# Performance work log

Measured on AMD Instinct MI355X. Metric: run time of the kernel, lower is better.

The kernel has to match this reference:

```python
import jax, jax.numpy as jnp
import numpy as np

S, B, D = 2048, 2, 1024   # seq_len, batch, d_model
H, Dh = 16, 64            # n_head, d_head (H*Dh == D)
LN_EPS = 1e-5


def _rel_shift(x):
    # x: [qlen, klen, bsz, n_head] -- standard Transformer-XL relative shift
    q, k, b, n = x.shape
    x = jnp.pad(x, ((0, 0), (1, 0), (0, 0), (0, 0)))  # [q, k+1, b, n]
    x = x.reshape(k + 1, q, b, n)[1:]                  # drop first row
    return x.reshape(q, k, b, n)


def setup_inputs() -> dict:
    key = jax.random.key(0)
    ks = jax.random.split(key, 8)
    s = 0.02
    return {
        "x":    jax.random.normal(ks[0], (S, B, D), jnp.float32),
        "r":    jax.random.normal(ks[1], (1, D), jnp.float32),          # learned pos vector
        "rw":   jax.random.normal(ks[2], (H, Dh), jnp.float32),          # content bias
        "rr":   jax.random.normal(ks[3], (H, Dh), jnp.float32),          # position bias
        "ln_g": jnp.ones((D,), jnp.float32),
        "ln_b": jnp.zeros((D,), jnp.float32),
        "Wqkv": jax.random.normal(ks[4], (D, 3 * H * Dh), jnp.float32) * s,
        "Wr":   jax.random.normal(ks[5], (D, H * Dh), jnp.float32) * s,
        "Wo":   jax.random.normal(ks[6], (H * Dh, D), jnp.float32) * s,
    }


def reference(x, r, rw, rr, ln_g, ln_b, Wqkv, Wr, Wo):
    # Pre-LayerNorm (dropout = identity in eval mode)
    mu = jnp.mean(x, axis=-1, keepdims=True)
    var = jnp.mean(jnp.square(x - mu), axis=-1, keepdims=True)
    xn = (x - mu) * jax.lax.rsqrt(var + LN_EPS) * ln_g + ln_b   # [S,B,D]

    # relative position input: r expanded over seq
    r_exp = jnp.broadcast_to(r, (S, D))                          # [S,D]

    qkv = xn @ Wqkv                                              # [S,B,3*H*Dh]
    q, k, v = jnp.split(qkv, 3, axis=-1)
    q = q.reshape(S, B, H, Dh)
    k = k.reshape(S, B, H, Dh)
    v = v.reshape(S, B, H, Dh)
    rk = (r_exp @ Wr).reshape(S, H, Dh)                          # [S,H,Dh]

    scale = 1.0 / np.sqrt(Dh).astype(np.float32)
    AC = jnp.einsum('ibnd,jbnd->ijbn', q + rw, k)                # content term
    BD = jnp.einsum('ibnd,jnd->ijbn', q + rr, rk)                # position term
    BD = _rel_shift(BD)
    attn = jax.nn.softmax((AC + BD) * scale, axis=1)             # over key axis j

    av = jnp.einsum('ijbn,jbnd->ibnd', attn, v).reshape(S, B, H * Dh)
    return xn + av @ Wo                                          # residual w/ normed input
```

## Files before the change

kernel.cpp:

```cpp
#include <hip/hip_runtime.h>

typedef unsigned short u16;
typedef __attribute__((ext_vector_type(8))) __bf16 bf16x8;
typedef __attribute__((ext_vector_type(8))) u16 u16x8;
typedef __attribute__((ext_vector_type(4))) float f32x4;
typedef __attribute__((ext_vector_type(16))) float f32x16;

__device__ __forceinline__ float bf2f(u16 u){
  union { unsigned int i; float f; } v; v.i = ((unsigned int)u) << 16; return v.f;
}
__device__ __forceinline__ u16 f2bf(float f){
  union { float f; unsigned int u; } v; v.f = f;
  unsigned int u = v.u;
  u += 0x7FFFu + ((u >> 16) & 1u);
  return (u16)(u >> 16);
}
__device__ __forceinline__ unsigned fbits(float f){
  union { float f; unsigned u; } v; v.f = f; return v.u;
}
__device__ __forceinline__ void gld_lds16(const u16* g, u16* l){
  __builtin_amdgcn_global_load_lds((const __attribute__((address_space(1))) unsigned int*)g,
                                   (__attribute__((address_space(3))) unsigned int*)l, 16, 0, 0);
}

__global__ __launch_bounds__(256) void prep_k(const float* __restrict__ Wqkv, u16* __restrict__ wqkvT,
                                              const float* __restrict__ Wo, u16* __restrict__ woT,
                                              const float* __restrict__ r, const float* __restrict__ Wr,
                                              float* __restrict__ rk0,
                                              const float* __restrict__ x, const float* __restrict__ gw,
                                              const float* __restrict__ bw, u16* __restrict__ xnb){
  __shared__ float tile[32][33];
  __shared__ float red[8];
  const int tx = threadIdx.x, ty = threadIdx.y;
  const int t = ty * 32 + tx;
  if(blockIdx.x == 128){
    const int n = blockIdx.y * 32 + (t & 31);
    const int chunk = t >> 5;
    float acc = 0.f;
    const int d0 = chunk * 128;
    for(int d = d0; d < d0 + 128; ++d)
      acc += r[d] * Wr[(size_t)d * 1024 + n];
    tile[chunk][t & 31] = acc;
    __syncthreads();
    if(chunk == 0){
      float s = 0.f;
      #pragma unroll
      for(int c = 0; c < 8; ++c) s += tile[c][t & 31];
      rk0[n] = s;
    }
    return;
  }
  if(blockIdx.x >= 129){
    const int row = (blockIdx.x - 129) * 32 + blockIdx.y;
    const float* xr = x + (size_t)row * 1024;
    float4 xv = *reinterpret_cast<const float4*>(xr + t * 4);
    float s  = xv.x + xv.y + xv.z + xv.w;
    float s2 = xv.x*xv.x + xv.y*xv.y + xv.z*xv.z + xv.w*xv.w;
    #pragma unroll
    for(int m = 1; m <= 32; m <<= 1){ s += __shfl_xor(s, m, 64); s2 += __shfl_xor(s2, m, 64); }
    const int w = t >> 6, lane = t & 63;
    if(lane == 0){ red[w] = s; red[4 + w] = s2; }
    __syncthreads();
    float S1 = red[0] + red[1] + red[2] + red[3];
    float S2 = red[4] + red[5] + red[6] + red[7];
    float mu = S1 * (1.f/1024.f);
    float var = S2 * (1.f/1024.f) - mu * mu;
    float rstd = rsqrtf(var + 1e-5f);
    float4 gv = *reinterpret_cast<const float4*>(gw + t * 4);
    float4 bv = *reinterpret_cast<const float4*>(bw + t * 4);
    ushort4 o;
    o.x = f2bf((xv.x - mu) * rstd * gv.x + bv.x);
    o.y = f2bf((xv.y - mu) * rstd * gv.y + bv.y);
    o.z = f2bf((xv.z - mu) * rstd * gv.z + bv.z);
    o.w = f2bf((xv.w - mu) * rstd * gv.w + bv.w);
    *reinterpret_cast<ushort4*>(xnb + (size_t)row * 1024 + t * 4) = o;
    return;
  }
  const float* in; u16* out; int C, bxx;
  if(blockIdx.x < 96){ in = Wqkv; out = wqkvT; C = 3072; bxx = blockIdx.x; }
  else               { in = Wo;   out = woT;   C = 1024; bxx = blockIdx.x - 96; }
  const int bx = bxx * 32, by = blockIdx.y * 32;
  #pragma unroll
  for(int i = 0; i < 32; i += 8)
    tile[ty + i][tx] = in[(size_t)(by + ty + i) * C + bx + tx];
  __syncthreads();
  #pragma unroll
  for(int i = 0; i < 32; i += 8)
    out[(size_t)(bx + ty + i) * 1024 + by + tx] = f2bf(tile[tx][ty + i]);
}

__global__ __launch_bounds__(256) void gemm_qkv_k(const u16* __restrict__ A, const u16* __restrict__ BT,
                                                  u16* __restrict__ Cb, u16* __restrict__ vT){
  __shared__ u16 sA[2][128 * 32];
  __shared__ u16 sB[2][128 * 32];
  __shared__ u16 tl[128 * 66];
  const int t = threadIdx.x;
  const int row0 = blockIdx.y * 128, col0 = blockIdx.x * 128;
  const int w = t >> 6, lane = t & 63, g = lane >> 4, lq = lane & 15;
  const int wr = (w >> 1) * 64, wc = (w & 1) * 64;
  const int K = 1024;
  f32x4 zero4 = {0.f, 0.f, 0.f, 0.f};
  f32x4 acc[4][4];
  #pragma unroll
  for(int mi = 0; mi < 4; ++mi)
    #pragma unroll
    for(int ni = 0; ni < 4; ++ni) acc[mi][ni] = zero4;

  for(int kt = 0; kt < K; kt += 64){
    #pragma unroll
    for(int ks = 0; ks < 2; ++ks){
      const int kk = kt + ks * 32;
      gld_lds16(A  + (size_t)(row0 +      (t >> 2)) * K + kk + (t & 3) * 8, &sA[ks][w * 512]);
      gld_lds16(A  + (size_t)(row0 + 64 + (t >> 2)) * K + kk + (t & 3) * 8, &sA[ks][2048 + w * 512]);
      gld_lds16(BT + (size_t)(col0 +      (t >> 2)) * K + kk + (t & 3) * 8, &sB[ks][w * 512]);
      gld_lds16(BT + (size_t)(col0 + 64 + (t >> 2)) * K + kk + (t & 3) * 8, &sB[ks][2048 + w * 512]);
    }
    __syncthreads();
    #pragma unroll
    for(int ks = 0; ks < 2; ++ks){
      bf16x8 af[4];
      #pragma unroll
      for(int mi = 0; mi < 4; ++mi)
        af[mi] = *reinterpret_cast<const bf16x8*>(&sA[ks][(wr + mi * 16 + lq) * 32 + g * 8]);
      #pragma unroll
      for(int ni = 0; ni < 4; ++ni){
        bf16x8 bfr = *reinterpret_cast<const bf16x8*>(&sB[ks][(wc + ni * 16 + lq) * 32 + g * 8]);
        #pragma unroll
        for(int mi = 0; mi < 4; ++mi)
          acc[mi][ni] = __builtin_amdgcn_mfma_f32_16x16x32_bf16(af[mi], bfr, acc[mi][ni], 0, 0, 0);
      }
    }
    __syncthreads();
  }
  if(blockIdx.x < 16){
    #pragma unroll
    for(int mi = 0; mi < 4; ++mi)
      #pragma unroll
      for(int ni = 0; ni < 4; ++ni)
        #pragma unroll
        for(int rg = 0; rg < 4; ++rg){
          const int row = row0 + wr + mi * 16 + g * 4 + rg;
          const int col = col0 + wc + ni * 16 + lq;
          Cb[(size_t)row * 2048 + col] = f2bf(acc[mi][ni][rg]);
        }
  } else {
    const int cv0 = col0 - 2048;
    #pragma unroll
    for(int half = 0; half < 2; ++half){
      if((w & 1) == half){
        #pragma unroll
        for(int mi = 0; mi < 4; ++mi)
          #pragma unroll
          for(int ni = 0; ni < 4; ++ni)
            #pragma unroll
            for(int rg = 0; rg < 4; ++rg)
              tl[(wr + mi * 16 + g * 4 + rg) * 66 + ni * 16 + lq] = f2bf(acc[mi][ni][rg]);
      }
      __syncthreads();
      const int h = (cv0 >> 6) + half;
      const int b2 = w >> 1, dup = w & 1, d = lane;
      const int R = (b2 * 16 + h) * 64 + d;
      u16 tmp[32];
      #pragma unroll
      for(int e = 0; e < 32; ++e)
        tmp[e] = tl[((dup * 32 + e) * 2 + b2) * 66 + d];
      u16* op = vT + (size_t)R * 2048 + (row0 >> 1) + dup * 32;
      *reinterpret_cast<u16x8*>(op)      = *reinterpret_cast<u16x8*>(&tmp[0]);
      *reinterpret_cast<u16x8*>(op + 8)  = *reinterpret_cast<u16x8*>(&tmp[8]);
      *reinterpret_cast<u16x8*>(op + 16) = *reinterpret_cast<u16x8*>(&tmp[16]);
      *reinterpret_cast<u16x8*>(op + 24) = *reinterpret_cast<u16x8*>(&tmp[24]);
      __syncthreads();
    }
  }
}

__global__ __launch_bounds__(256) void gemm_out_k(const u16* __restrict__ A, const u16* __restrict__ BT,
                                                  const u16* __restrict__ res, float* __restrict__ Cf){
  __shared__ u16 sA[128 * 32];
  __shared__ u16 sB[64 * 32];
  const int t = threadIdx.x;
  const int row0 = blockIdx.y * 128, col0 = blockIdx.x * 64;
  const int w = t >> 6, lane = t & 63, g = lane >> 4, lq = lane & 15;
  const int wr = (w >> 1) * 64, wc = (w & 1) * 32;
  const int K = 1024, N = 1024;
  f32x4 zero4 = {0.f, 0.f, 0.f, 0.f};
  f32x4 acc[4][2];
  #pragma unroll
  for(int mi = 0; mi < 4; ++mi)
    #pragma unroll
    for(int ni = 0; ni < 2; ++ni) acc[mi][ni] = zero4;

  for(int kt = 0; kt < K; kt += 32){
    gld_lds16(A  + (size_t)(row0 +      (t >> 2)) * K + kt + (t & 3) * 8, &sA[w * 512]);
    gld_lds16(A  + (size_t)(row0 + 64 + (t >> 2)) * K + kt + (t & 3) * 8, &sA[2048 + w * 512]);
    gld_lds16(BT + (size_t)(col0 +      (t >> 2)) * K + kt + (t & 3) * 8, &sB[w * 512]);
    __syncthreads();
    bf16x8 af[4];
    #pragma unroll
    for(int mi = 0; mi < 4; ++mi)
      af[mi] = *reinterpret_cast<const bf16x8*>(&sA[(wr + mi * 16 + lq) * 32 + g * 8]);
    #pragma unroll
    for(int ni = 0; ni < 2; ++ni){
      bf16x8 bfr = *reinterpret_cast<const bf16x8*>(&sB[(wc + ni * 16 + lq) * 32 + g * 8]);
      #pragma unroll
      for(int mi = 0; mi < 4; ++mi)
        acc[mi][ni] = __builtin_amdgcn_mfma_f32_16x16x32_bf16(af[mi], bfr, acc[mi][ni], 0, 0, 0);
    }
    __syncthreads();
  }
  #pragma unroll
  for(int mi = 0; mi < 4; ++mi)
    #pragma unroll
    for(int ni = 0; ni < 2; ++ni)
      #pragma unroll
      for(int rg = 0; rg < 4; ++rg){
        const int row = row0 + wr + mi * 16 + g * 4 + rg;
        const int col = col0 + wc + ni * 16 + lq;
        Cf[(size_t)row * N + col] = acc[mi][ni][rg] + bf2f(res[(size_t)row * N + col]);
      }
}

__global__ __launch_bounds__(256) void attn_k(const u16* __restrict__ qk, const u16* __restrict__ vT,
                                              const float* __restrict__ rw, const float* __restrict__ rr,
                                              const float* __restrict__ rk0, u16* __restrict__ av){
  constexpr int S = 2048, ST = 74;
  __shared__ u16 ks[2][64 * ST];
  __shared__ u16 vs[2][64 * ST];
  const int t = threadIdx.x;
  const int i0 = blockIdx.x * 128;
  const int bh = blockIdx.y;
  const int b = bh >> 4, h = bh & 15;
  const int w = t >> 6, lane = t & 63, m = lane & 31, q5 = lane >> 5;
  const int iw0 = i0 + w * 32;
  const int i_lane = iw0 + m;
  const float SC = 0.125f * 1.4426950408889634f;

  bf16x8 qf[4];
  float ciL, cpL;
  {
    const bool hasnext = (i_lane + 1 < S);
    const u16* qp  = qk + (size_t)(i_lane * 2 + b) * 2048 + h * 64;
    const u16* qp2 = qk + (size_t)((hasnext ? i_lane + 1 : i_lane) * 2 + b) * 2048 + h * 64;
    const float* rwp = rw  + h * 64;
    const float* rrp = rr  + h * 64;
    const float* rkp = rk0 + h * 64;
    float cpart = 0.f, cppart = 0.f;
    #pragma unroll
    for(int kt = 0; kt < 4; ++kt){
      const int dbase = kt * 16 + q5 * 8;
      u16x8 qv  = *reinterpret_cast<const u16x8*>(qp  + dbase);
      u16x8 qv2 = *reinterpret_cast<const u16x8*>(qp2 + dbase);
      u16x8 a;
      #pragma unroll
      for(int e = 0; e < 8; ++e){
        const float qe  = bf2f(qv[e]);
        const float rke = rkp[dbase + e];
        const float rre = rrp[dbase + e];
        a[e] = f2bf((qe + rwp[dbase + e]) * SC);
        cpart  += (qe + rre) * rke;
        cppart += (bf2f(qv2[e]) + rre) * rke;
      }
      qf[kt] = *reinterpret_cast<bf16x8*>(&a);
    }
    cpart  += __shfl_xor(cpart, 32, 64);
    cppart += __shfl_xor(cppart, 32, 64);
    ciL = cpart * SC;
    cpL = hasnext ? cppart * SC : 0.0f;
  }

  f32x16 acc0, acc1, z16;
  #pragma unroll
  for(int e = 0; e < 16; ++e) z16[e] = 0.f;
  acc0 = z16; acc1 = z16;
  float rsum = 0.f;

  const int jr = t >> 2, c0 = (t & 3) * 16;
  {
    const u16* kp = qk + (size_t)(jr * 2 + b) * 2048 + 1024 + h * 64 + c0;
    *reinterpret_cast<u16x8*>(&ks[0][jr * ST + c0])     = *reinterpret_cast<const u16x8*>(kp);
    *reinterpret_cast<u16x8*>(&ks[0][jr * ST + c0 + 8]) = *reinterpret_cast<const u16x8*>(kp + 8);
    const u16* vp = vT + ((size_t)bh * 64 + jr) * 2048 + c0;
    *reinterpret_cast<u16x8*>(&vs[0][jr * ST + c0])     = *reinterpret_cast<const u16x8*>(vp);
    *reinterpret_cast<u16x8*>(&vs[0][jr * ST + c0 + 8]) = *reinterpret_cast<const u16x8*>(vp + 8);
  }
  __syncthreads();

  for(int n = 0; n < 32; ++n){
    const int p = n & 1;
    u16x8 k0, k1, v0, v1;
    const bool pre = (n + 1 < 32);
    if(pre){
      const int j0n = (n + 1) * 64;
      const u16* kp = qk + (size_t)((j0n + jr) * 2 + b) * 2048 + 1024 + h * 64 + c0;
      k0 = *reinterpret_cast<const u16x8*>(kp);
      k1 = *reinterpret_cast<const u16x8*>(kp + 8);
      const u16* vp = vT + ((size_t)bh * 64 + jr) * 2048 + j0n + c0;
      v0 = *reinterpret_cast<const u16x8*>(vp);
      v1 = *reinterpret_cast<const u16x8*>(vp + 8);
    }
    const int j0 = n * 64;
    bf16x8 pfrag[4];
    #pragma unroll
    for(int jt = 0; jt < 2; ++jt){
      const int tj0 = j0 + jt * 32;
      f32x16 s = z16;
      #pragma unroll
      for(int kt = 0; kt < 4; ++kt){
        bf16x8 ka = *reinterpret_cast<const bf16x8*>(&ks[p][(jt * 32 + m) * ST + kt * 16 + q5 * 8]);
        s = __builtin_amdgcn_mfma_f32_32x32x16_bf16(ka, qf[kt], s, 0, 0, 0);
      }
      float pv[16];
      if(tj0 + 31 <= iw0){
        #pragma unroll
        for(int r2 = 0; r2 < 16; ++r2) pv[r2] = __builtin_amdgcn_exp2f(s[r2] + ciL);
      } else if(tj0 >= iw0 + 33){
        #pragma unroll
        for(int r2 = 0; r2 < 16; ++r2) pv[r2] = __builtin_amdgcn_exp2f(s[r2] + cpL);
      } else {
        #pragma unroll
        for(int r2 = 0; r2 < 16; ++r2){
          const int j = tj0 + (r2 & 3) + 8 * (r2 >> 2) + 4 * q5;
          const float t1 = (j <= i_lane) ? ciL : cpL;
          const float bdL = (j == i_lane + 1) ? 0.0f : t1;
          pv[r2] = __builtin_amdgcn_exp2f(s[r2] + bdL);
        }
      }
      #pragma unroll
      for(int r2 = 0; r2 < 16; ++r2) rsum += pv[r2];
      unsigned pk[8];
      #pragma unroll
      for(int q = 0; q < 8; ++q)
        pk[q] = __builtin_amdgcn_perm(fbits(pv[2 * q + 1]), fbits(pv[2 * q]), 0x07060302);
      unsigned sAx = (q5 == 0) ? pk[2] : pk[0];
      unsigned sAy = (q5 == 0) ? pk[3] : pk[1];
      unsigned rAx = (unsigned)__shfl_xor((int)sAx, 32, 64);
      unsigned rAy = (unsigned)__shfl_xor((int)sAy, 32, 64);
      unsigned sBx = (q5 == 0) ? pk[6] : pk[4];
      unsigned sBy = (q5 == 0) ? pk[7] : pk[5];
      unsigned rBx = (unsigned)__shfl_xor((int)sBx, 32, 64);
      unsigned rBy = (unsigned)__shfl_xor((int)sBy, 32, 64);
      union { unsigned u[4]; bf16x8 bf; } f0, f1;
      if(q5 == 0){
        f0.u[0] = pk[0]; f0.u[1] = pk[1]; f0.u[2] = rAx; f0.u[3] = rAy;
        f1.u[0] = pk[4]; f1.u[1] = pk[5]; f1.u[2] = rBx; f1.u[3] = rBy;
      } else {
        f0.u[0] = rAx; f0.u[1] = rAy; f0.u[2] = pk[2]; f0.u[3] = pk[3];
        f1.u[0] = rBx; f1.u[1] = rBy; f1.u[2] = pk[6]; f1.u[3] = pk[7];
      }
      pfrag[jt * 2 + 0] = f0.bf;
      pfrag[jt * 2 + 1] = f1.bf;
    }
    #pragma unroll
    for(int kt = 0; kt < 4; ++kt){
      bf16x8 va0 = *reinterpret_cast<const bf16x8*>(&vs[p][(m) * ST + kt * 16 + q5 * 8]);
      acc0 = __builtin_amdgcn_mfma_f32_32x32x16_bf16(va0, pfrag[kt], acc0, 0, 0, 0);
      bf16x8 va1 = *reinterpret_cast<const bf16x8*>(&vs[p][(32 + m) * ST + kt * 16 + q5 * 8]);
      acc1 = __builtin_amdgcn_mfma_f32_32x32x16_bf16(va1, pfrag[kt], acc1, 0, 0, 0);
    }
    if(pre){
      const int q2 = p ^ 1;
      *reinterpret_cast<u16x8*>(&ks[q2][jr * ST + c0])     = k0;
      *reinterpret_cast<u16x8*>(&ks[q2][jr * ST + c0 + 8]) = k1;
      *reinterpret_cast<u16x8*>(&vs[q2][jr * ST + c0])     = v0;
      *reinterpret_cast<u16x8*>(&vs[q2][jr * ST + c0 + 8]) = v1;
    }
    __syncthreads();
  }
  rsum += __shfl_xor(rsum, 32, 64);
  const float rinv = 1.0f / rsum;
  u16* op = av + (size_t)(i_lane * 2 + b) * 1024 + h * 64;
  #pragma unroll
  for(int dt = 0; dt < 2; ++dt){
    const f32x16& A = dt ? acc1 : acc0;
    #pragma unroll
    for(int rq = 0; rq < 4; ++rq){
      ushort4 o;
      o.x = f2bf(A[rq * 4 + 0] * rinv);
      o.y = f2bf(A[rq * 4 + 1] * rinv);
      o.z = f2bf(A[rq * 4 + 2] * rinv);
      o.w = f2bf(A[rq * 4 + 3] * rinv);
      const int d0 = dt * 32 + 8 * rq + 4 * q5;
      *reinterpret_cast<ushort4*>(op + d0) = o;
    }
  }
}

extern "C" void kernel_launch(void* const* d_in, const int* in_sizes, int n_in,
                              void* d_out, int out_size, void* d_ws, size_t ws_size,
                              hipStream_t stream){
  (void)in_sizes; (void)n_in; (void)out_size; (void)ws_size;
  const float* x    = (const float*)d_in[0];
  const float* r    = (const float*)d_in[1];
  const float* rw   = (const float*)d_in[2];
  const float* rr   = (const float*)d_in[3];
  const float* ln_g = (const float*)d_in[4];
  const float* ln_b = (const float*)d_in[5];
  const float* Wqkv = (const float*)d_in[6];
  const float* Wr   = (const float*)d_in[7];
  const float* Wo   = (const float*)d_in[8];
  char* ws = (char*)d_ws;
  u16*   xnb   = (u16*)(ws + 0);
  u16*   qk    = (u16*)(ws + 8388608);
  u16*   av    = (u16*)(ws + 25165824);
  u16*   woT   = (u16*)(ws + 33554432);
  u16*   wqkvT = (u16*)(ws + 35651584);
  u16*   vT    = (u16*)(ws + 41943040);
  float* rk0   = (float*)(ws + 50331648);
  float* out   = (float*)d_out;

  prep_k<<<dim3(257, 32), dim3(32, 8), 0, stream>>>(Wqkv, wqkvT, Wo, woT, r, Wr, rk0,
                                                    x, ln_g, ln_b, xnb);
  gemm_qkv_k<<<dim3(24, 32), 256, 0, stream>>>(xnb, wqkvT, qk, vT);
  attn_k<<<dim3(16, 32), 256, 0, stream>>>(qk, vT, rw, rr, rk0, av);
  gemm_out_k<<<dim3(16, 32), 256, 0, stream>>>(av, woT, xnb, out);
}
```

Before: 224.7 us.

## Split attention key range across two wave groups with LDS reduction

Doubles the attention block to 512 threads, with pairs of waves sharing the same 32 query rows and each handling alternate 64-key tiles. Partial accumulators and row sums from the odd-tile waves are combined through shared memory before normalisation. The aim is more waves in flight per query tile, giving better latency hiding and MFMA utilisation on a grid of only 512 blocks. In exchange, the double-buffered prefetch becomes a single buffer with an extra barrier per iteration, and there is a reduction step at the end.

```diff
diff --git a/kernel.cpp b/kernel.cpp
--- a/kernel.cpp
+++ b/kernel.cpp
@@ -220,18 +220,18 @@
       }
 }
 
-__global__ __launch_bounds__(256) void attn_k(const u16* __restrict__ qk, const u16* __restrict__ vT,
-                                              const float* __restrict__ rw, const float* __restrict__ rr,
-                                              const float* __restrict__ rk0, u16* __restrict__ av){
+__global__ __launch_bounds__(512, 4) void attn_k(const u16* __restrict__ qk, const u16* __restrict__ vT,
+                                                 const float* __restrict__ rw, const float* __restrict__ rr,
+                                                 const float* __restrict__ rk0, u16* __restrict__ av){
   constexpr int S = 2048, ST = 74;
-  __shared__ u16 ks[2][64 * ST];
-  __shared__ u16 vs[2][64 * ST];
+  __shared__ u16 smem[4][64 * ST];
   const int t = threadIdx.x;
   const int i0 = blockIdx.x * 128;
   const int bh = blockIdx.y;
   const int b = bh >> 4, h = bh & 15;
   const int w = t >> 6, lane = t & 63, m = lane & 31, q5 = lane >> 5;
-  const int iw0 = i0 + w * 32;
+  const int qw = w >> 1, kw = w & 1;
+  const int iw0 = i0 + qw * 32;
   const int i_lane = iw0 + m;
   const float SC = 0.125f * 1.4426950408889634f;
 
@@ -274,31 +274,34 @@
   acc0 = z16; acc1 = z16;
   float rsum = 0.f;
 
-  const int jr = t >> 2, c0 = (t & 3) * 16;
+  const int jr = t >> 3, c0 = (t & 7) * 8;
+  const int lo = jr * ST + c0;
   {
     const u16* kp = qk + (size_t)(jr * 2 + b) * 2048 + 1024 + h * 64 + c0;
-    *reinterpret_cast<u16x8*>(&ks[0][jr * ST + c0])     = *reinterpret_cast<const u16x8*>(kp);
-    *reinterpret_cast<u16x8*>(&ks[0][jr * ST + c0 + 8]) = *reinterpret_cast<const u16x8*>(kp + 8);
+    *reinterpret_cast<u16x8*>(&smem[0][lo]) = *reinterpret_cast<const u16x8*>(kp);
+    *reinterpret_cast<u16x8*>(&smem[1][lo]) = *reinterpret_cast<const u16x8*>(kp + (size_t)64 * 2 * 2048);
     const u16* vp = vT + ((size_t)bh * 64 + jr) * 2048 + c0;
-    *reinterpret_cast<u16x8*>(&vs[0][jr * ST + c0])     = *reinterpret_cast<const u16x8*>(vp);
-    *reinterpret_cast<u16x8*>(&vs[0][jr * ST + c0 + 8]) = *reinterpret_cast<const u16x8*>(vp + 8);
+    *reinterpret_cast<u16x8*>(&smem[2][lo]) = *reinterpret_cast<const u16x8*>(vp);
+    *reinterpret_cast<u16x8*>(&smem[3][lo]) = *reinterpret_cast<const u16x8*>(vp + 64);
   }
   __syncthreads();
 
-  for(int n = 0; n < 32; ++n){
-    const int p = n & 1;
-    u16x8 k0, k1, v0, v1;
-    const bool pre = (n + 1 < 32);
+  const u16* ksb = &smem[kw][0];
+  const u16* vsb = &smem[2 + kw][0];
+
+  for(int np = 0; np < 16; ++np){
+    u16x8 kE, kO, vE, vO;
+    const bool pre = (np + 1 < 16);
     if(pre){
-      const int j0n = (n + 1) * 64;
+      const int j0n = (2 * np + 2) * 64;
       const u16* kp = qk + (size_t)((j0n + jr) * 2 + b) * 2048 + 1024 + h * 64 + c0;
-      k0 = *reinterpret_cast<const u16x8*>(kp);
-      k1 = *reinterpret_cast<const u16x8*>(kp + 8);
+      kE = *reinterpret_cast<const u16x8*>(kp);
+      kO = *reinterpret_cast<const u16x8*>(kp + (size_t)64 * 2 * 2048);
       const u16* vp = vT + ((size_t)bh * 64 + jr) * 2048 + j0n + c0;
-      v0 = *reinterpret_cast<const u16x8*>(vp);
-      v1 = *reinterpret_cast<const u16x8*>(vp + 8);
-    }
-    const int j0 = n * 64;
+      vE = *reinterpret_cast<const u16x8*>(vp);
+      vO = *reinterpret_cast<const u16x8*>(vp + 64);
+    }
+    const int j0 = (2 * np + kw) * 64;
     bf16x8 pfrag[4];
     #pragma unroll
     for(int jt = 0; jt < 2; ++jt){
@@ -306,7 +309,7 @@
       f32x16 s = z16;
       #pragma unroll
       for(int kt = 0; kt < 4; ++kt){
-        bf16x8 ka = *reinterpret_cast<const bf16x8*>(&ks[p][(jt * 32 + m) * ST + kt * 16 + q5 * 8]);
+        bf16x8 ka = *reinterpret_cast<const bf16x8*>(&ksb[(jt * 32 + m) * ST + kt * 16 + q5 * 8]);
         s = __builtin_amdgcn_mfma_f32_32x32x16_bf16(ka, qf[kt], s, 0, 0, 0);
       }
       float pv[16];
@@ -352,35 +355,53 @@
     }
     #pragma unroll
     for(int kt = 0; kt < 4; ++kt){
-      bf16x8 va0 = *reinterpret_cast<const bf16x8*>(&vs[p][(m) * ST + kt * 16 + q5 * 8]);
+      bf16x8 va0 = *reinterpret_cast<const bf16x8*>(&vsb[(m) * ST + kt * 16 + q5 * 8]);
       acc0 = __builtin_amdgcn_mfma_f32_32x32x16_bf16(va0, pfrag[kt], acc0, 0, 0, 0);
-      bf16x8 va1 = *reinterpret_cast<const bf16x8*>(&vs[p][(32 + m) * ST + kt * 16 + q5 * 8]);
+      bf16x8 va1 = *reinterpret_cast<const bf16x8*>(&vsb[(32 + m) * ST + kt * 16 + q5 * 8]);
       acc1 = __builtin_amdgcn_mfma_f32_32x32x16_bf16(va1, pfrag[kt], acc1, 0, 0, 0);
     }
+    __syncthreads();
     if(pre){
-      const int q2 = p ^ 1;
-      *reinterpret_cast<u16x8*>(&ks[q2][jr * ST + c0])     = k0;
-      *reinterpret_cast<u16x8*>(&ks[q2][jr * ST + c0 + 8]) = k1;
-      *reinterpret_cast<u16x8*>(&vs[q2][jr * ST + c0])     = v0;
-      *reinterpret_cast<u16x8*>(&vs[q2][jr * ST + c0 + 8]) = v1;
-    }
-    __syncthreads();
-  }
+      *reinterpret_cast<u16x8*>(&smem[0][lo]) = kE;
+      *reinterpret_cast<u16x8*>(&smem[1][lo]) = kO;
+      *reinterpret_cast<u16x8*>(&smem[2][lo]) = vE;
+      *reinterpret_cast<u16x8*>(&smem[3][lo]) = vO;
+    }
+    __syncthreads();
+  }
+
   rsum += __shfl_xor(rsum, 32, 64);
-  const float rinv = 1.0f / rsum;
-  u16* op = av + (size_t)(i_lane * 2 + b) * 1024 + h * 64;
-  #pragma unroll
-  for(int dt = 0; dt < 2; ++dt){
-    const f32x16& A = dt ? acc1 : acc0;
-    #pragma unroll
-    for(int rq = 0; rq < 4; ++rq){
-      ushort4 o;
-      o.x = f2bf(A[rq * 4 + 0] * rinv);
-      o.y = f2bf(A[rq * 4 + 1] * rinv);
-      o.z = f2bf(A[rq * 4 + 2] * rinv);
-      o.w = f2bf(A[rq * 4 + 3] * rinv);
-      const int d0 = dt * 32 + 8 * rq + 4 * q5;
-      *reinterpret_cast<ushort4*>(op + d0) = o;
+
+  float* com = reinterpret_cast<float*>(&smem[0][0]) + (size_t)(qw * 64 + lane) * 33;
+  if(kw == 1){
+    #pragma unroll
+    for(int e = 0; e < 16; ++e) com[e] = acc0[e];
+    #pragma unroll
+    for(int e = 0; e < 16; ++e) com[16 + e] = acc1[e];
+    com[32] = rsum;
+  }
+  __syncthreads();
+  if(kw == 0){
+    #pragma unroll
+    for(int e = 0; e < 16; ++e) acc0[e] += com[e];
+    #pragma unroll
+    for(int e = 0; e < 16; ++e) acc1[e] += com[16 + e];
+    rsum += com[32];
+    const float rinv = 1.0f / rsum;
+    u16* op = av + (size_t)(i_lane * 2 + b) * 1024 + h * 64;
+    #pragma unroll
+    for(int dt = 0; dt < 2; ++dt){
+      const f32x16& A = dt ? acc1 : acc0;
+      #pragma unroll
+      for(int rq = 0; rq < 4; ++rq){
+        ushort4 o;
+        o.x = f2bf(A[rq * 4 + 0] * rinv);
+        o.y = f2bf(A[rq * 4 + 1] * rinv);
+        o.z = f2bf(A[rq * 4 + 2] * rinv);
+        o.w = f2bf(A[rq * 4 + 3] * rinv);
+        const int d0 = dt * 32 + 8 * rq + 4 * q5;
+        *reinterpret_cast<ushort4*>(op + d0) = o;
+      }
     }
   }
 }
@@ -411,6 +432,6 @@
   prep_k<<<dim3(257, 32), dim3(32, 8), 0, stream>>>(Wqkv, wqkvT, Wo, woT, r, Wr, rk0,
                                                     x, ln_g, ln_b, xnb);
   gemm_qkv_k<<<dim3(24, 32), 256, 0, stream>>>(xnb, wqkvT, qk, vT);
-  attn_k<<<dim3(16, 32), 256, 0, stream>>>(qk, vT, rw, rr, rk0, av);
+  attn_k<<<dim3(16, 32), 512, 0, stream>>>(qk, vT, rw, rr, rk0, av);
   gemm_out_k<<<dim3(16, 32), 256, 0, stream>>>(av, woT, xnb, out);
 }
```

Measured after the change: 315.3 us. 40.3% more time.

## Split attention key range across two blocks and combine partials in a separate kernel

Applied to the files above, without the earlier changes.

The attention kernel now takes a third grid dimension that splits the 32 key tiles into two halves. Each half writes unnormalised fp32 partial outputs and row sums to workspace, and a new comb_k kernel adds them, normalises and converts to bf16. The goal is to double the number of blocks so the GPU is better filled and latency is better hidden. The cost is extra global traffic for the fp32 partials, one more kernel launch, and an added __syncthreads per iteration. The split path only runs when the workspace is large enough.

```diff
diff --git a/kernel.cpp b/kernel.cpp
--- a/kernel.cpp
+++ b/kernel.cpp
@@ -222,13 +222,17 @@
 
 __global__ __launch_bounds__(256) void attn_k(const u16* __restrict__ qk, const u16* __restrict__ vT,
                                               const float* __restrict__ rw, const float* __restrict__ rr,
-                                              const float* __restrict__ rk0, u16* __restrict__ av){
+                                              const float* __restrict__ rk0, u16* __restrict__ av,
+                                              float* __restrict__ avp, float* __restrict__ rs){
   constexpr int S = 2048, ST = 74;
   __shared__ u16 ks[2][64 * ST];
   __shared__ u16 vs[2][64 * ST];
   const int t = threadIdx.x;
   const int i0 = blockIdx.x * 128;
   const int bh = blockIdx.y;
+  const int z = blockIdx.z;
+  const bool split = (gridDim.z == 2);
+  const int n0 = z * 16, nt = split ? 16 : 32;
   const int b = bh >> 4, h = bh & 15;
   const int w = t >> 6, lane = t & 63, m = lane & 31, q5 = lane >> 5;
   const int iw0 = i0 + w * 32;
@@ -276,19 +280,19 @@
 
   const int jr = t >> 2, c0 = (t & 3) * 16;
   {
-    const u16* kp = qk + (size_t)(jr * 2 + b) * 2048 + 1024 + h * 64 + c0;
+    const u16* kp = qk + (size_t)((n0 * 64 + jr) * 2 + b) * 2048 + 1024 + h * 64 + c0;
     *reinterpret_cast<u16x8*>(&ks[0][jr * ST + c0])     = *reinterpret_cast<const u16x8*>(kp);
     *reinterpret_cast<u16x8*>(&ks[0][jr * ST + c0 + 8]) = *reinterpret_cast<const u16x8*>(kp + 8);
-    const u16* vp = vT + ((size_t)bh * 64 + jr) * 2048 + c0;
+    const u16* vp = vT + ((size_t)bh * 64 + jr) * 2048 + n0 * 64 + c0;
     *reinterpret_cast<u16x8*>(&vs[0][jr * ST + c0])     = *reinterpret_cast<const u16x8*>(vp);
     *reinterpret_cast<u16x8*>(&vs[0][jr * ST + c0 + 8]) = *reinterpret_cast<const u16x8*>(vp + 8);
   }
   __syncthreads();
 
-  for(int n = 0; n < 32; ++n){
+  for(int n = n0; n < n0 + nt; ++n){
     const int p = n & 1;
     u16x8 k0, k1, v0, v1;
-    const bool pre = (n + 1 < 32);
+    const bool pre = (n + 1 < n0 + nt);
     if(pre){
       const int j0n = (n + 1) * 64;
       const u16* kp = qk + (size_t)((j0n + jr) * 2 + b) * 2048 + 1024 + h * 64 + c0;
@@ -357,6 +361,7 @@
       bf16x8 va1 = *reinterpret_cast<const bf16x8*>(&vs[p][(32 + m) * ST + kt * 16 + q5 * 8]);
       acc1 = __builtin_amdgcn_mfma_f32_32x32x16_bf16(va1, pfrag[kt], acc1, 0, 0, 0);
     }
+    __syncthreads();
     if(pre){
       const int q2 = p ^ 1;
       *reinterpret_cast<u16x8*>(&ks[q2][jr * ST + c0])     = k0;
@@ -367,28 +372,63 @@
     __syncthreads();
   }
   rsum += __shfl_xor(rsum, 32, 64);
-  const float rinv = 1.0f / rsum;
-  u16* op = av + (size_t)(i_lane * 2 + b) * 1024 + h * 64;
-  #pragma unroll
-  for(int dt = 0; dt < 2; ++dt){
-    const f32x16& A = dt ? acc1 : acc0;
-    #pragma unroll
-    for(int rq = 0; rq < 4; ++rq){
-      ushort4 o;
-      o.x = f2bf(A[rq * 4 + 0] * rinv);
-      o.y = f2bf(A[rq * 4 + 1] * rinv);
-      o.z = f2bf(A[rq * 4 + 2] * rinv);
-      o.w = f2bf(A[rq * 4 + 3] * rinv);
-      const int d0 = dt * 32 + 8 * rq + 4 * q5;
-      *reinterpret_cast<ushort4*>(op + d0) = o;
-    }
-  }
+  if(split){
+    float* op = avp + (size_t)z * 4194304 + ((size_t)(i_lane * 2 + b) * 16 + h) * 64;
+    #pragma unroll
+    for(int dt = 0; dt < 2; ++dt){
+      const f32x16& A = dt ? acc1 : acc0;
+      #pragma unroll
+      for(int rq = 0; rq < 4; ++rq){
+        float4 o;
+        o.x = A[rq * 4 + 0]; o.y = A[rq * 4 + 1]; o.z = A[rq * 4 + 2]; o.w = A[rq * 4 + 3];
+        const int d0 = dt * 32 + 8 * rq + 4 * q5;
+        *reinterpret_cast<float4*>(op + d0) = o;
+      }
+    }
+    if(q5 == 0) rs[(size_t)z * 65536 + (size_t)(i_lane * 2 + b) * 16 + h] = rsum;
+  } else {
+    const float rinv = 1.0f / rsum;
+    u16* op = av + (size_t)(i_lane * 2 + b) * 1024 + h * 64;
+    #pragma unroll
+    for(int dt = 0; dt < 2; ++dt){
+      const f32x16& A = dt ? acc1 : acc0;
+      #pragma unroll
+      for(int rq = 0; rq < 4; ++rq){
+        ushort4 o;
+        o.x = f2bf(A[rq * 4 + 0] * rinv);
+        o.y = f2bf(A[rq * 4 + 1] * rinv);
+        o.z = f2bf(A[rq * 4 + 2] * rinv);
+        o.w = f2bf(A[rq * 4 + 3] * rinv);
+        const int d0 = dt * 32 + 8 * rq + 4 * q5;
+        *reinterpret_cast<ushort4*>(op + d0) = o;
+      }
+    }
+  }
+}
+
+__global__ __launch_bounds__(256) void comb_k(const float* __restrict__ avp, const float* __restrict__ rs,
+                                              u16* __restrict__ av){
+  const int gid = blockIdx.x * 256 + threadIdx.x;
+  const size_t i8 = (size_t)gid * 8;
+  const size_t rowh = i8 >> 6;
+  const float rinv = 1.0f / (rs[rowh] + rs[65536 + rowh]);
+  const float4 a0 = *reinterpret_cast<const float4*>(avp + i8);
+  const float4 a1 = *reinterpret_cast<const float4*>(avp + i8 + 4);
+  const float4 b0 = *reinterpret_cast<const float4*>(avp + 4194304 + i8);
+  const float4 b1 = *reinterpret_cast<const float4*>(avp + 4194304 + i8 + 4);
+  ushort4 o0, o1;
+  o0.x = f2bf((a0.x + b0.x) * rinv); o0.y = f2bf((a0.y + b0.y) * rinv);
+  o0.z = f2bf((a0.z + b0.z) * rinv); o0.w = f2bf((a0.w + b0.w) * rinv);
+  o1.x = f2bf((a1.x + b1.x) * rinv); o1.y = f2bf((a1.y + b1.y) * rinv);
+  o1.z = f2bf((a1.z + b1.z) * rinv); o1.w = f2bf((a1.w + b1.w) * rinv);
+  *reinterpret_cast<ushort4*>(av + i8)     = o0;
+  *reinterpret_cast<ushort4*>(av + i8 + 4) = o1;
 }
 
 extern "C" void kernel_launch(void* const* d_in, const int* in_sizes, int n_in,
                               void* d_out, int out_size, void* d_ws, size_t ws_size,
                               hipStream_t stream){
-  (void)in_sizes; (void)n_in; (void)out_size; (void)ws_size;
+  (void)in_sizes; (void)n_in; (void)out_size;
   const float* x    = (const float*)d_in[0];
   const float* r    = (const float*)d_in[1];
   const float* rw   = (const float*)d_in[2];
@@ -406,11 +446,19 @@
   u16*   wqkvT = (u16*)(ws + 35651584);
   u16*   vT    = (u16*)(ws + 41943040);
   float* rk0   = (float*)(ws + 50331648);
+  float* rs    = (float*)(ws + 50335744);
+  float* avp   = (float*)(ws + 50860032);
   float* out   = (float*)d_out;
+  const bool split = ws_size >= (size_t)84414464;
 
   prep_k<<<dim3(257, 32), dim3(32, 8), 0, stream>>>(Wqkv, wqkvT, Wo, woT, r, Wr, rk0,
                                                     x, ln_g, ln_b, xnb);
   gemm_qkv_k<<<dim3(24, 32), 256, 0, stream>>>(xnb, wqkvT, qk, vT);
-  attn_k<<<dim3(16, 32), 256, 0, stream>>>(qk, vT, rw, rr, rk0, av);
+  if(split){
+    attn_k<<<dim3(16, 32, 2), 256, 0, stream>>>(qk, vT, rw, rr, rk0, av, avp, rs);
+    comb_k<<<dim3(2048), 256, 0, stream>>>(avp, rs, av);
+  } else {
+    attn_k<<<dim3(16, 32, 1), 256, 0, stream>>>(qk, vT, rw, rr, rk0, av, avp, rs);
+  }
   gemm_out_k<<<dim3(16, 32), 256, 0, stream>>>(av, woT, xnb, out);
 }
```

After: 235.2 us. +4.7%, slower.

## Software-pipeline attention: overlap next tile QK^T/softmax with current PV MFMAs

Applied to the files above, without the earlier changes.

Restructures the attention inner loop so the QK^T scores and softmax of tile n+1 are computed while the PV MFMAs of tile n issue. Global K/V loads now prefetch two tiles ahead, which needs an extra barrier per iteration before the LDS buffer is overwritten. It also adds a launch-bounds occupancy hint of 2 blocks per SM. The aim is to hide exp and softmax latency behind matrix work, at the cost of more live registers and an extra __syncthreads.

```diff
diff --git a/kernel.cpp b/kernel.cpp
--- a/kernel.cpp
+++ b/kernel.cpp
@@ -220,9 +220,9 @@
       }
 }
 
-__global__ __launch_bounds__(256) void attn_k(const u16* __restrict__ qk, const u16* __restrict__ vT,
-                                              const float* __restrict__ rw, const float* __restrict__ rr,
-                                              const float* __restrict__ rk0, u16* __restrict__ av){
+__global__ __launch_bounds__(256, 2) void attn_k(const u16* __restrict__ qk, const u16* __restrict__ vT,
+                                                 const float* __restrict__ rw, const float* __restrict__ rr,
+                                                 const float* __restrict__ rk0, u16* __restrict__ av){
   constexpr int S = 2048, ST = 74;
   __shared__ u16 ks[2][64 * ST];
   __shared__ u16 vs[2][64 * ST];
@@ -275,40 +275,39 @@
   float rsum = 0.f;
 
   const int jr = t >> 2, c0 = (t & 3) * 16;
-  {
-    const u16* kp = qk + (size_t)(jr * 2 + b) * 2048 + 1024 + h * 64 + c0;
-    *reinterpret_cast<u16x8*>(&ks[0][jr * ST + c0])     = *reinterpret_cast<const u16x8*>(kp);
-    *reinterpret_cast<u16x8*>(&ks[0][jr * ST + c0 + 8]) = *reinterpret_cast<const u16x8*>(kp + 8);
-    const u16* vp = vT + ((size_t)bh * 64 + jr) * 2048 + c0;
-    *reinterpret_cast<u16x8*>(&vs[0][jr * ST + c0])     = *reinterpret_cast<const u16x8*>(vp);
-    *reinterpret_cast<u16x8*>(&vs[0][jr * ST + c0 + 8]) = *reinterpret_cast<const u16x8*>(vp + 8);
+  #pragma unroll
+  for(int tile = 0; tile < 2; ++tile){
+    const u16* kp = qk + (size_t)((tile * 64 + jr) * 2 + b) * 2048 + 1024 + h * 64 + c0;
+    *reinterpret_cast<u16x8*>(&ks[tile][jr * ST + c0])     = *reinterpret_cast<const u16x8*>(kp);
+    *reinterpret_cast<u16x8*>(&ks[tile][jr * ST + c0 + 8]) = *reinterpret_cast<const u16x8*>(kp + 8);
+    const u16* vp = vT + ((size_t)bh * 64 + jr) * 2048 + tile * 64 + c0;
+    *reinterpret_cast<u16x8*>(&vs[tile][jr * ST + c0])     = *reinterpret_cast<const u16x8*>(vp);
+    *reinterpret_cast<u16x8*>(&vs[tile][jr * ST + c0 + 8]) = *reinterpret_cast<const u16x8*>(vp + 8);
   }
   __syncthreads();
 
-  for(int n = 0; n < 32; ++n){
-    const int p = n & 1;
-    u16x8 k0, k1, v0, v1;
-    const bool pre = (n + 1 < 32);
-    if(pre){
-      const int j0n = (n + 1) * 64;
-      const u16* kp = qk + (size_t)((j0n + jr) * 2 + b) * 2048 + 1024 + h * 64 + c0;
-      k0 = *reinterpret_cast<const u16x8*>(kp);
-      k1 = *reinterpret_cast<const u16x8*>(kp + 8);
-      const u16* vp = vT + ((size_t)bh * 64 + jr) * 2048 + j0n + c0;
-      v0 = *reinterpret_cast<const u16x8*>(vp);
-      v1 = *reinterpret_cast<const u16x8*>(vp + 8);
-    }
-    const int j0 = n * 64;
-    bf16x8 pfrag[4];
+  bf16x8 pfrag[4];
+  f32x16 sj[2];
+
+  auto qk_phase = [&](int tile){
+    const u16* base = &ks[tile & 1][0];
+    #pragma unroll
+    for(int jt = 0; jt < 2; ++jt){
+      f32x16 s = z16;
+      #pragma unroll
+      for(int kt = 0; kt < 4; ++kt){
+        bf16x8 ka = *reinterpret_cast<const bf16x8*>(&base[(jt * 32 + m) * ST + kt * 16 + q5 * 8]);
+        s = __builtin_amdgcn_mfma_f32_32x32x16_bf16(ka, qf[kt], s, 0, 0, 0);
+      }
+      sj[jt] = s;
+    }
+  };
+  auto sm_phase = [&](int tile){
+    const int j0 = tile * 64;
     #pragma unroll
     for(int jt = 0; jt < 2; ++jt){
       const int tj0 = j0 + jt * 32;
-      f32x16 s = z16;
-      #pragma unroll
-      for(int kt = 0; kt < 4; ++kt){
-        bf16x8 ka = *reinterpret_cast<const bf16x8*>(&ks[p][(jt * 32 + m) * ST + kt * 16 + q5 * 8]);
-        s = __builtin_amdgcn_mfma_f32_32x32x16_bf16(ka, qf[kt], s, 0, 0, 0);
-      }
+      f32x16 s = sj[jt];
       float pv[16];
       if(tj0 + 31 <= iw0){
         #pragma unroll
@@ -350,6 +349,26 @@
       pfrag[jt * 2 + 0] = f0.bf;
       pfrag[jt * 2 + 1] = f1.bf;
     }
+  };
+
+  qk_phase(0);
+  sm_phase(0);
+
+  for(int n = 0; n < 32; ++n){
+    const int p = n & 1;
+    u16x8 k0, k1, v0, v1;
+    const bool pre = (n + 2 < 32);
+    if(pre){
+      const int j0n = (n + 2) * 64;
+      const u16* kp = qk + (size_t)((j0n + jr) * 2 + b) * 2048 + 1024 + h * 64 + c0;
+      k0 = *reinterpret_cast<const u16x8*>(kp);
+      k1 = *reinterpret_cast<const u16x8*>(kp + 8);
+      const u16* vp = vT + ((size_t)bh * 64 + jr) * 2048 + j0n + c0;
+      v0 = *reinterpret_cast<const u16x8*>(vp);
+      v1 = *reinterpret_cast<const u16x8*>(vp + 8);
+    }
+    const bool more = (n + 1 < 32);
+    if(more) qk_phase(n + 1);
     #pragma unroll
     for(int kt = 0; kt < 4; ++kt){
       bf16x8 va0 = *reinterpret_cast<const bf16x8*>(&vs[p][(m) * ST + kt * 16 + q5 * 8]);
@@ -357,12 +376,13 @@
       bf16x8 va1 = *reinterpret_cast<const bf16x8*>(&vs[p][(32 + m) * ST + kt * 16 + q5 * 8]);
       acc1 = __builtin_amdgcn_mfma_f32_32x32x16_bf16(va1, pfrag[kt], acc1, 0, 0, 0);
     }
+    if(more) sm_phase(n + 1);
+    __syncthreads();
     if(pre){
-      const int q2 = p ^ 1;
-      *reinterpret_cast<u16x8*>(&ks[q2][jr * ST + c0])     = k0;
-      *reinterpret_cast<u16x8*>(&ks[q2][jr * ST + c0 + 8]) = k1;
-      *reinterpret_cast<u16x8*>(&vs[q2][jr * ST + c0])     = v0;
-      *reinterpret_cast<u16x8*>(&vs[q2][jr * ST + c0 + 8]) = v1;
+      *reinterpret_cast<u16x8*>(&ks[p][jr * ST + c0])     = k0;
+      *reinterpret_cast<u16x8*>(&ks[p][jr * ST + c0 + 8]) = k1;
+      *reinterpret_cast<u16x8*>(&vs[p][jr * ST + c0])     = v0;
+      *reinterpret_cast<u16x8*>(&vs[p][jr * ST + c0 + 8]) = v1;
     }
     __syncthreads();
   }
```

Result: slower. 259.0 us (+15.3%).
